# Performance work log

Hardware: AMD Instinct MI355X
Metric: run time of the kernel (lower is better)

## Reference

```python
import jax, jax.numpy as jnp
import numpy as np

B, T, D = 2, 4096, 512
H, W = 8, 32
HD = D // H            # 64
HIDDEN = 3 * D         # SwiGLU expansion = 3
SCALE = float(np.sqrt(HD))
EPS = 1e-5


def setup_inputs() -> dict:
    key = jax.random.key(0)
    ks = jax.random.split(key, 8)
    s = 0.02  # small init for weight matrices
    return {
        "x": jax.random.normal(ks[0], (B, T, D), dtype=jnp.float32),
        "pre_g": jnp.ones((D,), jnp.float32), "pre_b": jnp.zeros((D,), jnp.float32),
        "wq": jax.random.normal(ks[1], (D, D), jnp.float32) * s,
        "wkv": jax.random.normal(ks[2], (D, 2 * D), jnp.float32) * s,
        "wo": jax.random.normal(ks[3], (D, D), jnp.float32) * s,
        "attn_g": jnp.ones((D,), jnp.float32), "attn_b": jnp.zeros((D,), jnp.float32),
        "freqs": jax.random.normal(ks[4], (D,), jnp.float32) * 0.02,
        "phases": jnp.zeros((D,), jnp.float32),
        "amp": jnp.full((1,), 0.1, jnp.float32),
        "w_gate": jax.random.normal(ks[5], (D, HIDDEN), jnp.float32) * s,
        "w_val": jax.random.normal(ks[6], (D, HIDDEN), jnp.float32) * s,
        "w_proj": jax.random.normal(ks[7], (HIDDEN, D), jnp.float32) * s,
        "ffn_g": jnp.ones((D,), jnp.float32), "ffn_b": jnp.zeros((D,), jnp.float32),
    }


def _ln(x, g, b):
    mu = jnp.mean(x, axis=-1, keepdims=True)
    var = jnp.mean(jnp.square(x - mu), axis=-1, keepdims=True)
    return (x - mu) * jax.lax.rsqrt(var + EPS) * g + b


def _gather_window(z):
    # z: (B, T, H, C) -> nb: (B, T, W, H, C) with nb[:, t, w] = z[:, t-1-w] (zeros if t-1-w < 0)
    zp = jnp.pad(z, ((0, 0), (W, 0), (0, 0), (0, 0)))
    idx = jnp.arange(T)[:, None] + (W - 1) - jnp.arange(W)[None, :]  # (T, W), values in [0, T+W-1)
    return zp[:, idx]  # (B, T, W, H, C)


def reference(x, pre_g, pre_b, wq, wkv, wo, attn_g, attn_b,
              freqs, phases, amp, w_gate, w_val, w_proj, ffn_g, ffn_b):
    h = _ln(x, pre_g, pre_b)

    # ---- multi-head causal tension (sigmoid local attention) ----
    q = (h @ wq).reshape(B, T, H, HD)
    kv = (h @ wkv).reshape(B, T, H, 2 * HD)
    nb_kv = _gather_window(kv)                     # (B, T, W, H, 2*HD)
    nb_k, nb_v = nb_kv[..., :HD], nb_kv[..., HD:]
    tau = jax.nn.sigmoid(jnp.einsum('bthd,btwhd->bthw', q, nb_k) / SCALE)
    msg = jnp.einsum('bthw,btwhd->bthd', tau, nb_v).reshape(B, T, D)
    h = _ln(h + msg @ wo, attn_g, attn_b)

    # ---- oscillatory modulation ----
    pos = jnp.arange(T, dtype=jnp.float32)[:, None]  # (T, 1)
    mod = jnp.sin(pos * freqs + phases)              # (T, D)
    y = h * (1.0 + amp * mod)[None]

    # ---- SwiGLU FFN ----
    z = (jax.nn.silu(y @ w_gate) * (y @ w_val)) @ w_proj
    return _ln(y + z, ffn_g, ffn_b)
```

## Files before the change

### kernel.cpp

```cpp
#include <hip/hip_runtime.h>
#include <hip/hip_bf16.h>
#include <math.h>

#define T_LEN   4096
#define D_DIM   512
#define H_NUM   8
#define HD_DIM  64
#define W_WIN   32
#define HID_DIM 1536
#define M_ROWS  8192
#define QKV_LD  1536
#define BK 64

typedef __hip_bfloat16 bf16;
typedef __bf16  bf16x8 __attribute__((ext_vector_type(8)));
typedef float   f32x4  __attribute__((ext_vector_type(4)));

#define G_AS __attribute__((address_space(1)))
#define L_AS __attribute__((address_space(3)))

#define SBAR()        __builtin_amdgcn_s_barrier()
#define SCHED_FENCE() __builtin_amdgcn_sched_barrier(0)
#define WAIT_VM(N)    asm volatile("s_waitcnt vmcnt(" #N ")" ::: "memory")
#define WAIT_LGKM0()  asm volatile("s_waitcnt lgkmcnt(0)" ::: "memory")

__device__ __forceinline__ float b2f(bf16 x) { return __bfloat162float(x); }
__device__ __forceinline__ bf16  f2b(float x){ return __float2bfloat16(x); }

__device__ __forceinline__ void gload_lds16(const bf16* g, bf16* l) {
  __builtin_amdgcn_global_load_lds((const G_AS unsigned int*)g,
                                   (L_AS unsigned int*)l, 16, 0, 0);
}

__device__ __forceinline__ float rdP(const void* p, int i, bool f32) {
  return f32 ? ((const float*)p)[i] : b2f(((const bf16*)p)[i]);
}

__device__ __forceinline__ float wave_reduce_sum(float v) {
  #pragma unroll
  for (int off = 32; off; off >>= 1) v += __shfl_xor(v, off, 64);
  return v;
}

__device__ __forceinline__ bool detect_f32(const unsigned* __restrict__ x) {
  int lane = threadIdx.x & 63;
  int votes = 0;
  #pragma unroll
  for (int i = 0; i < 4; ++i) {
    unsigned e = (x[lane * 4 + i] >> 7) & 0xffu;
    votes += (e >= 90u && e <= 140u) ? 1 : 0;
  }
  float v = wave_reduce_sum((float)votes);
  return v < 200.f;
}

__device__ __forceinline__ void swizzle_xy(int gx, int& bx, int& by) {
  int lid = blockIdx.x;
  int sub = lid & 7;
  int grp = lid >> 3;
  bx = grp % gx;
  by = (grp / gx) * 8 + sub;
}

__global__ __launch_bounds__(256) void ln_kernel(
    const void* __restrict__ in, const void* __restrict__ g, const void* __restrict__ bb,
    void* __restrict__ out, int mode,
    const void* __restrict__ freqs, const void* __restrict__ phases,
    const void* __restrict__ amp,
    const unsigned* __restrict__ xdet, int in_follows, int out_follows)
{
  bool f32  = detect_f32(xdet);
  bool inF  = f32 && (in_follows != 0);
  bool outF = f32 && (out_follows != 0);

  int wave = threadIdx.x >> 6;
  int lane = threadIdx.x & 63;
  int row  = blockIdx.x * 4 + wave;

  float x[8];
  if (inF) {
    const float* rp = (const float*)in + (size_t)row * D_DIM + lane * 8;
    float4 v0 = *reinterpret_cast<const float4*>(rp);
    float4 v1 = *reinterpret_cast<const float4*>(rp + 4);
    x[0]=v0.x; x[1]=v0.y; x[2]=v0.z; x[3]=v0.w;
    x[4]=v1.x; x[5]=v1.y; x[6]=v1.z; x[7]=v1.w;
  } else {
    bf16x8 v = *reinterpret_cast<const bf16x8*>(
        (const bf16*)in + (size_t)row * D_DIM + lane * 8);
    #pragma unroll
    for (int i = 0; i < 8; ++i) x[i] = (float)v[i];
  }

  float s = 0.f, s2 = 0.f;
  #pragma unroll
  for (int i = 0; i < 8; ++i) { s += x[i]; s2 += x[i]*x[i]; }
  s  = wave_reduce_sum(s);
  s2 = wave_reduce_sum(s2);
  float mu   = s * (1.f / D_DIM);
  float var  = s2 * (1.f / D_DIM) - mu * mu;
  float rstd = rsqrtf(var + 1e-5f);

  int t = row & (T_LEN - 1);
  float ampf = (mode == 1) ? rdP(amp, 0, f32) : 0.f;

  float o[8];
  #pragma unroll
  for (int i = 0; i < 8; ++i) {
    int d = lane * 8 + i;
    float val = (x[i] - mu) * rstd * rdP(g, d, f32) + rdP(bb, d, f32);
    if (mode == 1) {
      float m = sinf(fmaf((float)t, rdP(freqs, d, f32), rdP(phases, d, f32)));
      val *= (1.f + ampf * m);
    }
    o[i] = val;
  }

  if (outF) {
    float* op = (float*)out + (size_t)row * D_DIM + lane * 8;
    *reinterpret_cast<float4*>(op)     = make_float4(o[0], o[1], o[2], o[3]);
    *reinterpret_cast<float4*>(op + 4) = make_float4(o[4], o[5], o[6], o[7]);
  } else {
    bf16x8 ov;
    #pragma unroll
    for (int i = 0; i < 8; ++i) ov[i] = (__bf16)o[i];
    *reinterpret_cast<bf16x8*>((bf16*)out + (size_t)row * D_DIM + lane * 8) = ov;
  }
}

__global__ __launch_bounds__(256) void prep_kernel(
    const void* s0, const void* s1, const void* s2, const void* s3,
    const void* s4, const void* s5,
    bf16* d0, bf16* d1, bf16* d2, bf16* d3, bf16* d4, bf16* d5,
    const void* __restrict__ xin, const void* __restrict__ pre_g,
    const void* __restrict__ pre_b, bf16* __restrict__ hout,
    const unsigned* __restrict__ xdet)
{
  __shared__ bf16 tile[32][33];
  bool f32 = detect_f32(xdet);
  int bid = blockIdx.x;

  if (bid >= 3328) {
    int wave = threadIdx.x >> 6;
    int lane = threadIdx.x & 63;
    int row  = (bid - 3328) * 4 + wave;

    float x[8];
    if (f32) {
      const float* rp = (const float*)xin + (size_t)row * D_DIM + lane * 8;
      float4 v0 = *reinterpret_cast<const float4*>(rp);
      float4 v1 = *reinterpret_cast<const float4*>(rp + 4);
      x[0]=v0.x; x[1]=v0.y; x[2]=v0.z; x[3]=v0.w;
      x[4]=v1.x; x[5]=v1.y; x[6]=v1.z; x[7]=v1.w;
    } else {
      bf16x8 v = *reinterpret_cast<const bf16x8*>(
          (const bf16*)xin + (size_t)row * D_DIM + lane * 8);
      #pragma unroll
      for (int i = 0; i < 8; ++i) x[i] = (float)v[i];
    }

    float s = 0.f, s2 = 0.f;
    #pragma unroll
    for (int i = 0; i < 8; ++i) { s += x[i]; s2 += x[i]*x[i]; }
    s  = wave_reduce_sum(s);
    s2 = wave_reduce_sum(s2);
    float mu   = s * (1.f / D_DIM);
    float var  = s2 * (1.f / D_DIM) - mu * mu;
    float rstd = rsqrtf(var + 1e-5f);

    bf16x8 ov;
    #pragma unroll
    for (int i = 0; i < 8; ++i) {
      int d = lane * 8 + i;
      ov[i] = (__bf16)((x[i] - mu) * rstd * rdP(pre_g, d, f32) + rdP(pre_b, d, f32));
    }
    *reinterpret_cast<bf16x8*>(hout + (size_t)row * D_DIM + lane * 8) = ov;
    return;
  }

  const void* src; bf16* dst; int R, C, lid, tiles_x;
  if      (bid < 256)  { src=s0; dst=d0; R=512;  C=512;  lid=bid;      tiles_x=16; }
  else if (bid < 768)  { src=s1; dst=d1; R=512;  C=1024; lid=bid-256;  tiles_x=32; }
  else if (bid < 1024) { src=s2; dst=d2; R=512;  C=512;  lid=bid-768;  tiles_x=16; }
  else if (bid < 1792) { src=s3; dst=d3; R=512;  C=1536; lid=bid-1024; tiles_x=48; }
  else if (bid < 2560) { src=s4; dst=d4; R=512;  C=1536; lid=bid-1792; tiles_x=48; }
  else                 { src=s5; dst=d5; R=1536; C=512;  lid=bid-2560; tiles_x=16; }

  int tx = threadIdx.x & 31;
  int ty = threadIdx.x >> 5;
  int c0 = (lid % tiles_x) * 32;
  int r0 = (lid / tiles_x) * 32;
  #pragma unroll
  for (int j = 0; j < 32; j += 8)
    tile[ty + j][tx] = f2b(rdP(src, (size_t)(r0 + ty + j) * C + c0 + tx, f32));
  __syncthreads();
  #pragma unroll
  for (int j = 0; j < 32; j += 8)
    dst[(size_t)(c0 + ty + j) * R + r0 + tx] = tile[tx][ty + j];
}

template<int BNT, bool DBUF>
__global__ __launch_bounds__(256) void gemm_tile_kernel(
    const bf16* __restrict__ A, const bf16* __restrict__ Bt,
    bf16* Cout, const bf16* extra, int N, int K, int lda, int mode, int gx)
{
  constexpr int BJ  = BNT / 32;
  constexpr int NB  = DBUF ? 2 : 1;
  constexpr int ASZ = 128 * BK;
  constexpr int BSZ = BNT * BK;
  constexpr int CPF = BNT + 4;
  constexpr int CPB = BNT + 8;
  constexpr size_t STAGE = (size_t)NB * (ASZ + BSZ) * 2;
  constexpr size_t CTSZ  = (BNT == 64) ? (size_t)128 * CPF * 4 : (size_t)128 * CPB * 2;
  constexpr size_t SMEMSZ = STAGE > CTSZ ? STAGE : CTSZ;
  __shared__ alignas(16) char smem[SMEMSZ];
  bf16* Asb = (bf16*)smem;
  bf16* Bsb = Asb + (size_t)NB * ASZ;

  int bx, by; swizzle_xy(gx, bx, by);
  int mbase = by * 128, nbase = bx * BNT;
  int tid  = threadIdx.x;
  int lane = tid & 63;
  int wid  = tid >> 6;
  int quad = lane >> 4, l16 = lane & 15;
  int wm = (wid >> 1) * 64, wn = (wid & 1) * (BNT / 2);

  int srow = tid >> 3;
  int scol = (tid & 7) ^ (srow & 7);
  const bf16* Ag = A  + (size_t)(mbase + srow) * lda + scol * 8;
  const bf16* Bg = Bt + (size_t)(nbase + srow) * K   + scol * 8;

  f32x4 acc[4][BJ] = {};
  int nk = K / BK;

  auto compute = [&](int cb) {
    #pragma unroll
    for (int ko = 0; ko < 2; ++ko) {
      bf16x8 a[4], b[BJ];
      int c = ((ko * 4 + quad) ^ (l16 & 7)) * 8;
      #pragma unroll
      for (int i = 0; i < 4; ++i)
        a[i] = *reinterpret_cast<const bf16x8*>(&Asb[cb * ASZ + (wm + i * 16 + l16) * BK + c]);
      #pragma unroll
      for (int j = 0; j < BJ; ++j)
        b[j] = *reinterpret_cast<const bf16x8*>(&Bsb[cb * BSZ + (wn + j * 16 + l16) * BK + c]);
      #pragma unroll
      for (int i = 0; i < 4; ++i)
        #pragma unroll
        for (int j = 0; j < BJ; ++j)
          acc[i][j] = __builtin_amdgcn_mfma_f32_16x16x32_bf16(a[i], b[j], acc[i][j], 0, 0, 0);
    }
  };

  if constexpr (DBUF) {
    #pragma unroll
    for (int j = 0; j < 4; ++j)
      gload_lds16(Ag + (size_t)(j * 32) * lda, &Asb[j * 2048 + tid * 8]);
    #pragma unroll
    for (int j = 0; j < BJ; ++j)
      gload_lds16(Bg + (size_t)(j * 32) * K,   &Bsb[j * 2048 + tid * 8]);
    Ag += BK; Bg += BK;

    for (int t = 0; t < nk; ++t) {
      int cur = t & 1;
      if (t + 1 < nk) {
        int nxt = cur ^ 1;
        #pragma unroll
        for (int j = 0; j < 4; ++j)
          gload_lds16(Ag + (size_t)(j * 32) * lda, &Asb[nxt * ASZ + j * 2048 + tid * 8]);
        #pragma unroll
        for (int j = 0; j < BJ; ++j)
          gload_lds16(Bg + (size_t)(j * 32) * K,   &Bsb[nxt * BSZ + j * 2048 + tid * 8]);
        Ag += BK; Bg += BK;
        if constexpr (BNT == 128) { WAIT_VM(8); } else { WAIT_VM(6); }
      } else {
        WAIT_VM(0);
      }
      SBAR();
      SCHED_FENCE();

      compute(cur);

      WAIT_LGKM0();
      SBAR();
      SCHED_FENCE();
    }
  } else {
    for (int t = 0; t < nk; ++t) {
      __syncthreads();
      #pragma unroll
      for (int j = 0; j < 4; ++j)
        gload_lds16(Ag + (size_t)(j * 32) * lda, &Asb[j * 2048 + tid * 8]);
      #pragma unroll
      for (int j = 0; j < BJ; ++j)
        gload_lds16(Bg + (size_t)(j * 32) * K,   &Bsb[j * 2048 + tid * 8]);
      Ag += BK; Bg += BK;
      __syncthreads();

      compute(0);
    }
    __syncthreads();
  }

  if constexpr (BNT == 64) {
    float* CT = (float*)smem;
    #pragma unroll
    for (int i = 0; i < 4; ++i)
      #pragma unroll
      for (int j = 0; j < 2; ++j)
        #pragma unroll
        for (int r = 0; r < 4; ++r)
          CT[(wm + i * 16 + quad * 4 + r) * CPF + wn + j * 16 + l16] = acc[i][j][r];
    __syncthreads();
    #pragma unroll
    for (int p = 0; p < 4; ++p) {
      int row = (tid >> 3) + p * 32;
      int c8  = tid & 7;
      const float* rp = &CT[row * CPF + c8 * 8];
      float4 v0 = *reinterpret_cast<const float4*>(rp);
      float4 v1 = *reinterpret_cast<const float4*>(rp + 4);
      float vv[8] = {v0.x, v0.y, v0.z, v0.w, v1.x, v1.y, v1.z, v1.w};
      size_t gidx = (size_t)(mbase + row) * N + nbase + c8 * 8;
      if (mode == 1) {
        bf16x8 e = *reinterpret_cast<const bf16x8*>(extra + gidx);
        #pragma unroll
        for (int k2 = 0; k2 < 8; ++k2) vv[k2] += (float)e[k2];
      }
      bf16x8 ov;
      #pragma unroll
      for (int k2 = 0; k2 < 8; ++k2) ov[k2] = (__bf16)vv[k2];
      *reinterpret_cast<bf16x8*>(Cout + gidx) = ov;
    }
  } else {
    bf16* CT = (bf16*)smem;
    #pragma unroll
    for (int i = 0; i < 4; ++i)
      #pragma unroll
      for (int j = 0; j < BJ; ++j)
        #pragma unroll
        for (int r = 0; r < 4; ++r)
          CT[(wm + i * 16 + quad * 4 + r) * CPB + wn + j * 16 + l16] = f2b(acc[i][j][r]);
    __syncthreads();
    #pragma unroll
    for (int p = 0; p < 8; ++p) {
      int row = (tid >> 4) + p * 16;
      int c16 = tid & 15;
      bf16x8 ov = *reinterpret_cast<const bf16x8*>(&CT[row * CPB + c16 * 8]);
      *reinterpret_cast<bf16x8*>(Cout + (size_t)(mbase + row) * N + nbase + c16 * 8) = ov;
    }
  }
}

__global__ __launch_bounds__(256) void gateval_kernel(
    const bf16* __restrict__ A, const bf16* __restrict__ Btg,
    const bf16* __restrict__ Btv, bf16* __restrict__ Cout,
    int N, int K, int lda, int gx)
{
  constexpr int CP = 72;
  __shared__ alignas(16) char smem[2 * (16384 + 8192 + 8192)];
  bf16* Asb = (bf16*)smem;
  bf16* Bgs = Asb + 2 * 8192;
  bf16* Bvs = Bgs + 2 * 4096;

  int bx, by; swizzle_xy(gx, bx, by);
  int mbase = by * 128, nbase = bx * 64;
  int tid  = threadIdx.x;
  int lane = tid & 63;
  int wid  = tid >> 6;
  int quad = lane >> 4, l16 = lane & 15;
  int wm = (wid >> 1) * 64, wn = (wid & 1) * 32;

  int srow = tid >> 3;
  int scol = (tid & 7) ^ (srow & 7);
  const bf16* Ag = A   + (size_t)(mbase + srow) * lda + scol * 8;
  const bf16* Gg = Btg + (size_t)(nbase + srow) * K   + scol * 8;
  const bf16* Vg = Btv + (size_t)(nbase + srow) * K   + scol * 8;

  f32x4 accg[4][2] = {};
  f32x4 accv[4][2] = {};
  int nk = K / BK;

  #pragma unroll
  for (int j = 0; j < 4; ++j)
    gload_lds16(Ag + (size_t)(j * 32) * lda, &Asb[j * 2048 + tid * 8]);
  #pragma unroll
  for (int j = 0; j < 2; ++j) {
    gload_lds16(Gg + (size_t)(j * 32) * K, &Bgs[j * 2048 + tid * 8]);
    gload_lds16(Vg + (size_t)(j * 32) * K, &Bvs[j * 2048 + tid * 8]);
  }
  Ag += BK; Gg += BK; Vg += BK;

  for (int t = 0; t < nk; ++t) {
    int cur = t & 1;
    if (t + 1 < nk) {
      int nxt = cur ^ 1;
      #pragma unroll
      for (int j = 0; j < 4; ++j)
        gload_lds16(Ag + (size_t)(j * 32) * lda, &Asb[nxt * 8192 + j * 2048 + tid * 8]);
      #pragma unroll
      for (int j = 0; j < 2; ++j) {
        gload_lds16(Gg + (size_t)(j * 32) * K, &Bgs[nxt * 4096 + j * 2048 + tid * 8]);
        gload_lds16(Vg + (size_t)(j * 32) * K, &Bvs[nxt * 4096 + j * 2048 + tid * 8]);
      }
      Ag += BK; Gg += BK; Vg += BK;
      WAIT_VM(8);
    } else {
      WAIT_VM(0);
    }
    SBAR();
    SCHED_FENCE();

    #pragma unroll
    for (int ko = 0; ko < 2; ++ko) {
      bf16x8 a[4], bg[2], bv[2];
      int c = ((ko * 4 + quad) ^ (l16 & 7)) * 8;
      #pragma unroll
      for (int i = 0; i < 4; ++i)
        a[i]  = *reinterpret_cast<const bf16x8*>(&Asb[cur * 8192 + (wm + i * 16 + l16) * BK + c]);
      #pragma unroll
      for (int j = 0; j < 2; ++j) {
        bg[j] = *reinterpret_cast<const bf16x8*>(&Bgs[cur * 4096 + (wn + j * 16 + l16) * BK + c]);
        bv[j] = *reinterpret_cast<const bf16x8*>(&Bvs[cur * 4096 + (wn + j * 16 + l16) * BK + c]);
      }
      #pragma unroll
      for (int i = 0; i < 4; ++i)
        #pragma unroll
        for (int j = 0; j < 2; ++j) {
          accg[i][j] = __builtin_amdgcn_mfma_f32_16x16x32_bf16(a[i], bg[j], accg[i][j], 0, 0, 0);
          accv[i][j] = __builtin_amdgcn_mfma_f32_16x16x32_bf16(a[i], bv[j], accv[i][j], 0, 0, 0);
        }
    }

    WAIT_LGKM0();
    SBAR();
    SCHED_FENCE();
  }

  bf16* CT = (bf16*)smem;
  #pragma unroll
  for (int i = 0; i < 4; ++i)
    #pragma unroll
    for (int j = 0; j < 2; ++j)
      #pragma unroll
      for (int r = 0; r < 4; ++r) {
        float g = accg[i][j][r];
        float v = accv[i][j][r];
        CT[(wm + i * 16 + quad * 4 + r) * CP + wn + j * 16 + l16] =
            f2b(g / (1.f + expf(-g)) * v);
      }
  __syncthreads();
  #pragma unroll
  for (int p = 0; p < 4; ++p) {
    int row = (tid >> 3) + p * 32;
    int c8  = tid & 7;
    bf16x8 ov = *reinterpret_cast<const bf16x8*>(&CT[row * CP + c8 * 8]);
    *reinterpret_cast<bf16x8*>(Cout + (size_t)(mbase + row) * N + nbase + c8 * 8) = ov;
  }
}

#define VT_BYTES 9216
#define PL_BYTES 2304
#define ATTN_SET (VT_BYTES + PL_BYTES)
__device__ __forceinline__ int vt_addr(int d, int t) { return d * 144 + t * 2; }

__global__ __launch_bounds__(256) void attn_mfma_kernel(bf16* qkv)
{
  __shared__ alignas(16) char lds_raw[4 * ATTN_SET];
  int lane = threadIdx.x & 63;
  int widx = threadIdx.x >> 6;
  int u    = blockIdx.x * 4 + widx;
  int tile = u >> 3, head = u & 7;
  int rowbase = tile * 16;
  int t0   = rowbase & (T_LEN - 1);
  int l16  = lane & 15, quad = lane >> 4;

  char* wbase = lds_raw + widx * ATTN_SET;
  char* Vl = wbase;
  bf16* Pl = (bf16*)(wbase + VT_BYTES);

  #pragma unroll
  for (int it = 0; it < 6; ++it) {
    int chunk = it * 64 + lane;
    int t  = chunk >> 3;
    int dc = chunk & 7;
    int row = rowbase - 32 + t;
    if (row < 0) row = 0;
    bf16x8 v = *reinterpret_cast<const bf16x8*>(
        qkv + (size_t)row * QKV_LD + 512 + head * 128 + 64 + dc * 8);
    #pragma unroll
    for (int jj = 0; jj < 8; ++jj)
      *(bf16*)(Vl + vt_addr(dc * 8 + jj, t)) = (bf16)(__bf16)v[jj];
  }
  bf16x8 z = {};
  *reinterpret_cast<bf16x8*>(Vl + vt_addr(lane, 48)) = z;
  *reinterpret_cast<bf16x8*>(Vl + vt_addr(lane, 56)) = z;

  bf16x8 aq0, aq1;
  {
    const bf16* qrow = qkv + (size_t)(rowbase + l16) * QKV_LD + head * HD_DIM + quad * 8;
    aq0 = *reinterpret_cast<const bf16x8*>(qrow);
    aq1 = *reinterpret_cast<const bf16x8*>(qrow + 32);
  }

  f32x4 sacc[3] = {};
  #pragma unroll
  for (int jt = 0; jt < 3; ++jt) {
    int tok = rowbase - 32 + jt * 16 + l16;
    if (tok < 0) tok = 0;
    const bf16* krow = qkv + (size_t)tok * QKV_LD + 512 + head * 128 + quad * 8;
    bf16x8 b0 = *reinterpret_cast<const bf16x8*>(krow);
    bf16x8 b1 = *reinterpret_cast<const bf16x8*>(krow + 32);
    sacc[jt] = __builtin_amdgcn_mfma_f32_16x16x32_bf16(aq0, b0, sacc[jt], 0, 0, 0);
    sacc[jt] = __builtin_amdgcn_mfma_f32_16x16x32_bf16(aq1, b1, sacc[jt], 0, 0, 0);
  }

  #pragma unroll
  for (int jt = 0; jt < 3; ++jt) {
    int j = jt * 16 + l16;
    #pragma unroll
    for (int r = 0; r < 4; ++r) {
      int i = quad * 4 + r;
      bool valid = (j >= i) && (j <= i + 31) && (t0 - 32 + j >= 0);
      float tau = valid ? 1.f / (1.f + expf(-sacc[jt][r] * 0.125f)) : 0.f;
      Pl[i * 72 + j] = f2b(tau);
    }
  }
  #pragma unroll
  for (int r = 0; r < 4; ++r) Pl[(quad * 4 + r) * 72 + 48 + l16] = f2b(0.f);

  __syncthreads();

  bf16x8 ap0 = *reinterpret_cast<const bf16x8*>((char*)Pl + l16 * 144 + quad * 16);
  bf16x8 ap1 = *reinterpret_cast<const bf16x8*>((char*)Pl + l16 * 144 + 64 + quad * 16);

  f32x4 macc[4] = {};
  #pragma unroll
  for (int nt = 0; nt < 4; ++nt) {
    int d = nt * 16 + l16;
    bf16x8 bv0 = *reinterpret_cast<const bf16x8*>(Vl + vt_addr(d, quad * 8));
    bf16x8 bv1 = *reinterpret_cast<const bf16x8*>(Vl + vt_addr(d, 32 + quad * 8));
    macc[nt] = __builtin_amdgcn_mfma_f32_16x16x32_bf16(ap0, bv0, macc[nt], 0, 0, 0);
    macc[nt] = __builtin_amdgcn_mfma_f32_16x16x32_bf16(ap1, bv1, macc[nt], 0, 0, 0);
  }

  #pragma unroll
  for (int nt = 0; nt < 4; ++nt)
    #pragma unroll
    for (int r = 0; r < 4; ++r)
      Pl[(quad * 4 + r) * 72 + nt * 16 + l16] = f2b(macc[nt][r]);

  #pragma unroll
  for (int p = 0; p < 2; ++p) {
    int row = (lane >> 3) + p * 8;
    int c8  = lane & 7;
    bf16x8 ov = *reinterpret_cast<const bf16x8*>(&Pl[row * 72 + c8 * 8]);
    *reinterpret_cast<bf16x8*>(
        qkv + (size_t)(rowbase + row) * QKV_LD + head * HD_DIM + c8 * 8) = ov;
  }
}

extern "C" void kernel_launch(void* const* d_in, const int* in_sizes, int n_in,
                              void* d_out, int out_size, void* d_ws, size_t ws_size,
                              hipStream_t stream)
{
  const void* x      = d_in[0];
  const void* pre_g  = d_in[1];
  const void* pre_b  = d_in[2];
  const void* wq     = d_in[3];
  const void* wkv    = d_in[4];
  const void* wo     = d_in[5];
  const void* attn_g = d_in[6];
  const void* attn_b = d_in[7];
  const void* freqs  = d_in[8];
  const void* phases = d_in[9];
  const void* amp    = d_in[10];
  const void* w_gate = d_in[11];
  const void* w_val  = d_in[12];
  const void* w_proj = d_in[13];
  const void* ffn_g  = d_in[14];
  const void* ffn_b  = d_in[15];
  const unsigned* xdet = (const unsigned*)x;

  char* ws = (char*)d_ws;
  bf16* Btqkv = (bf16*)(ws + 512);
  bf16* Bto   = (bf16*)(ws + 1573376);
  bf16* Btg   = (bf16*)(ws + 2097664);
  bf16* Btv   = (bf16*)(ws + 3670528);
  bf16* Btp   = (bf16*)(ws + 5243392);
  bf16* h     = (bf16*)(ws + 6816256);
  bf16* qkvb  = (bf16*)(ws + 15204864);
  bf16* gb    = qkvb;

  prep_kernel<<<5376, 256, 0, stream>>>(
      wq, wkv, wo, w_gate, w_val, w_proj,
      Btqkv, Btqkv + 512 * 512, Bto, Btg, Btv, Btp,
      x, pre_g, pre_b, h, xdet);

  gemm_tile_kernel<128, false><<<768, 256, 0, stream>>>(h, Btqkv, qkvb, nullptr,
                                                        1536, 512, 512, 0, 12);

  attn_mfma_kernel<<<1024, 256, 0, stream>>>(qkvb);

  gemm_tile_kernel<64, true><<<512, 256, 0, stream>>>(qkvb, Bto, h, h,
                                                      512, 512, QKV_LD, 1, 8);

  ln_kernel<<<2048, 256, 0, stream>>>(h, attn_g, attn_b, h, 1,
                                      freqs, phases, amp, xdet, 0, 0);

  gateval_kernel<<<1536, 256, 0, stream>>>(h, Btg, Btv, gb,
                                           1536, 512, 512, 24);

  gemm_tile_kernel<64, true><<<512, 256, 0, stream>>>(gb, Btp, h, h,
                                                      512, 1536, QKV_LD, 1, 8);

  ln_kernel<<<2048, 256, 0, stream>>>(h, ffn_g, ffn_b, d_out, 0,
                                      nullptr, nullptr, nullptr, xdet, 0, 1);
}
```

Measured before the change: 274.3 us.

## Use 512-thread blocks for GEMM kernels and switch to fast sine

The GEMM and gate/value kernels now run with 512 threads (8 waves) per block on the same output tile. Each wave gets a smaller sub-tile with fewer accumulators, and the global-to-LDS staging and epilogue loops are re-split so each thread issues fewer loads. The aim is more waves in flight to hide memory latency and lower register pressure, at the cost of less reuse per wave and more LDS reads per MFMA. The oscillatory modulation also swaps sinf for __sinf, which is cheaper but less accurate when t*freq is large.

```diff
diff --git a/kernel.cpp b/kernel.cpp
--- a/kernel.cpp
+++ b/kernel.cpp
@@ -109,7 +109,7 @@
     int d = lane * 8 + i;
     float val = (x[i] - mu) * rstd * rdP(g, d, f32) + rdP(bb, d, f32);
     if (mode == 1) {
-      float m = sinf(fmaf((float)t, rdP(freqs, d, f32), rdP(phases, d, f32)));
+      float m = __sinf(fmaf((float)t, rdP(freqs, d, f32), rdP(phases, d, f32)));
       val *= (1.f + ampf * m);
     }
     o[i] = val;
@@ -199,16 +199,17 @@
 }
 
 template<int BNT, bool DBUF>
-__global__ __launch_bounds__(256) void gemm_tile_kernel(
+__global__ __launch_bounds__(512) void gemm_tile_kernel(
     const bf16* __restrict__ A, const bf16* __restrict__ Bt,
     bf16* Cout, const bf16* extra, int N, int K, int lda, int mode, int gx)
 {
-  constexpr int BJ  = BNT / 32;
+  constexpr int MI  = (BNT == 128) ? 4 : 2;
+  constexpr int NJ  = 2;
   constexpr int NB  = DBUF ? 2 : 1;
   constexpr int ASZ = 128 * BK;
   constexpr int BSZ = BNT * BK;
-  constexpr int CPF = BNT + 4;
-  constexpr int CPB = BNT + 8;
+  constexpr int CPF = 68;
+  constexpr int CPB = 136;
   constexpr size_t STAGE = (size_t)NB * (ASZ + BSZ) * 2;
   constexpr size_t CTSZ  = (BNT == 64) ? (size_t)128 * CPF * 4 : (size_t)128 * CPB * 2;
   constexpr size_t SMEMSZ = STAGE > CTSZ ? STAGE : CTSZ;
@@ -222,56 +223,56 @@
   int lane = tid & 63;
   int wid  = tid >> 6;
   int quad = lane >> 4, l16 = lane & 15;
-  int wm = (wid >> 1) * 64, wn = (wid & 1) * (BNT / 2);
-
-  int srow = tid >> 3;
-  int scol = (tid & 7) ^ (srow & 7);
-  const bf16* Ag = A  + (size_t)(mbase + srow) * lda + scol * 8;
-  const bf16* Bg = Bt + (size_t)(nbase + srow) * K   + scol * 8;
-
-  f32x4 acc[4][BJ] = {};
+  int wm, wn;
+  if constexpr (BNT == 128) { wm = (wid >> 2) * 64; wn = (wid & 3) * 32; }
+  else                      { wm = (wid >> 1) * 32; wn = (wid & 1) * 32; }
+
+  int srow  = tid >> 3;
+  int scolb = ((tid & 7) ^ (srow & 7)) * 8;
+  const bf16* Ag = A  + (size_t)(mbase + srow) * lda + scolb;
+  const bf16* Bg = Bt + (size_t)(nbase + srow) * K   + scolb;
+
+  f32x4 acc[MI][NJ] = {};
   int nk = K / BK;
 
+  auto stage = [&](int buf) {
+    gload_lds16(Ag,                    &Asb[buf * ASZ + tid * 8]);
+    gload_lds16(Ag + (size_t)64 * lda, &Asb[buf * ASZ + tid * 8 + 4096]);
+    if constexpr (BNT == 128) {
+      gload_lds16(Bg,                  &Bsb[buf * BSZ + tid * 8]);
+      gload_lds16(Bg + (size_t)64 * K, &Bsb[buf * BSZ + tid * 8 + 4096]);
+    } else {
+      gload_lds16(Bg,                  &Bsb[buf * BSZ + tid * 8]);
+    }
+    Ag += BK; Bg += BK;
+  };
+
   auto compute = [&](int cb) {
     #pragma unroll
     for (int ko = 0; ko < 2; ++ko) {
-      bf16x8 a[4], b[BJ];
+      bf16x8 a[MI], b[NJ];
       int c = ((ko * 4 + quad) ^ (l16 & 7)) * 8;
       #pragma unroll
-      for (int i = 0; i < 4; ++i)
+      for (int i = 0; i < MI; ++i)
         a[i] = *reinterpret_cast<const bf16x8*>(&Asb[cb * ASZ + (wm + i * 16 + l16) * BK + c]);
       #pragma unroll
-      for (int j = 0; j < BJ; ++j)
+      for (int j = 0; j < NJ; ++j)
         b[j] = *reinterpret_cast<const bf16x8*>(&Bsb[cb * BSZ + (wn + j * 16 + l16) * BK + c]);
       #pragma unroll
-      for (int i = 0; i < 4; ++i)
+      for (int i = 0; i < MI; ++i)
         #pragma unroll
-        for (int j = 0; j < BJ; ++j)
+        for (int j = 0; j < NJ; ++j)
           acc[i][j] = __builtin_amdgcn_mfma_f32_16x16x32_bf16(a[i], b[j], acc[i][j], 0, 0, 0);
     }
   };
 
   if constexpr (DBUF) {
-    #pragma unroll
-    for (int j = 0; j < 4; ++j)
-      gload_lds16(Ag + (size_t)(j * 32) * lda, &Asb[j * 2048 + tid * 8]);
-    #pragma unroll
-    for (int j = 0; j < BJ; ++j)
-      gload_lds16(Bg + (size_t)(j * 32) * K,   &Bsb[j * 2048 + tid * 8]);
-    Ag += BK; Bg += BK;
-
+    stage(0);
     for (int t = 0; t < nk; ++t) {
       int cur = t & 1;
       if (t + 1 < nk) {
-        int nxt = cur ^ 1;
-        #pragma unroll
-        for (int j = 0; j < 4; ++j)
-          gload_lds16(Ag + (size_t)(j * 32) * lda, &Asb[nxt * ASZ + j * 2048 + tid * 8]);
-        #pragma unroll
-        for (int j = 0; j < BJ; ++j)
-          gload_lds16(Bg + (size_t)(j * 32) * K,   &Bsb[nxt * BSZ + j * 2048 + tid * 8]);
-        Ag += BK; Bg += BK;
-        if constexpr (BNT == 128) { WAIT_VM(8); } else { WAIT_VM(6); }
+        stage(cur ^ 1);
+        if constexpr (BNT == 128) { WAIT_VM(4); } else { WAIT_VM(3); }
       } else {
         WAIT_VM(0);
       }
@@ -287,15 +288,8 @@
   } else {
     for (int t = 0; t < nk; ++t) {
       __syncthreads();
-      #pragma unroll
-      for (int j = 0; j < 4; ++j)
-        gload_lds16(Ag + (size_t)(j * 32) * lda, &Asb[j * 2048 + tid * 8]);
-      #pragma unroll
-      for (int j = 0; j < BJ; ++j)
-        gload_lds16(Bg + (size_t)(j * 32) * K,   &Bsb[j * 2048 + tid * 8]);
-      Ag += BK; Bg += BK;
+      stage(0);
       __syncthreads();
-
       compute(0);
     }
     __syncthreads();
@@ -304,16 +298,16 @@
   if constexpr (BNT == 64) {
     float* CT = (float*)smem;
     #pragma unroll
-    for (int i = 0; i < 4; ++i)
-      #pragma unroll
-      for (int j = 0; j < 2; ++j)
+    for (int i = 0; i < MI; ++i)
+      #pragma unroll
+      for (int j = 0; j < NJ; ++j)
         #pragma unroll
         for (int r = 0; r < 4; ++r)
           CT[(wm + i * 16 + quad * 4 + r) * CPF + wn + j * 16 + l16] = acc[i][j][r];
     __syncthreads();
     #pragma unroll
-    for (int p = 0; p < 4; ++p) {
-      int row = (tid >> 3) + p * 32;
+    for (int p = 0; p < 2; ++p) {
+      int row = (tid >> 3) + p * 64;
       int c8  = tid & 7;
       const float* rp = &CT[row * CPF + c8 * 8];
       float4 v0 = *reinterpret_cast<const float4*>(rp);
@@ -333,16 +327,16 @@
   } else {
     bf16* CT = (bf16*)smem;
     #pragma unroll
-    for (int i = 0; i < 4; ++i)
-      #pragma unroll
-      for (int j = 0; j < BJ; ++j)
+    for (int i = 0; i < MI; ++i)
+      #pragma unroll
+      for (int j = 0; j < NJ; ++j)
         #pragma unroll
         for (int r = 0; r < 4; ++r)
           CT[(wm + i * 16 + quad * 4 + r) * CPB + wn + j * 16 + l16] = f2b(acc[i][j][r]);
     __syncthreads();
     #pragma unroll
-    for (int p = 0; p < 8; ++p) {
-      int row = (tid >> 4) + p * 16;
+    for (int p = 0; p < 4; ++p) {
+      int row = (tid >> 4) + p * 32;
       int c16 = tid & 15;
       bf16x8 ov = *reinterpret_cast<const bf16x8*>(&CT[row * CPB + c16 * 8]);
       *reinterpret_cast<bf16x8*>(Cout + (size_t)(mbase + row) * N + nbase + c16 * 8) = ov;
@@ -350,7 +344,7 @@
   }
 }
 
-__global__ __launch_bounds__(256) void gateval_kernel(
+__global__ __launch_bounds__(512) void gateval_kernel(
     const bf16* __restrict__ A, const bf16* __restrict__ Btg,
     const bf16* __restrict__ Btv, bf16* __restrict__ Cout,
     int N, int K, int lda, int gx)
@@ -367,42 +361,32 @@
   int lane = tid & 63;
   int wid  = tid >> 6;
   int quad = lane >> 4, l16 = lane & 15;
-  int wm = (wid >> 1) * 64, wn = (wid & 1) * 32;
-
-  int srow = tid >> 3;
-  int scol = (tid & 7) ^ (srow & 7);
-  const bf16* Ag = A   + (size_t)(mbase + srow) * lda + scol * 8;
-  const bf16* Gg = Btg + (size_t)(nbase + srow) * K   + scol * 8;
-  const bf16* Vg = Btv + (size_t)(nbase + srow) * K   + scol * 8;
-
-  f32x4 accg[4][2] = {};
-  f32x4 accv[4][2] = {};
+  int wm = (wid >> 1) * 32, wn = (wid & 1) * 32;
+
+  int srow  = tid >> 3;
+  int scolb = ((tid & 7) ^ (srow & 7)) * 8;
+  const bf16* Ag = A   + (size_t)(mbase + srow) * lda + scolb;
+  const bf16* Gg = Btg + (size_t)(nbase + srow) * K   + scolb;
+  const bf16* Vg = Btv + (size_t)(nbase + srow) * K   + scolb;
+
+  f32x4 accg[2][2] = {};
+  f32x4 accv[2][2] = {};
   int nk = K / BK;
 
-  #pragma unroll
-  for (int j = 0; j < 4; ++j)
-    gload_lds16(Ag + (size_t)(j * 32) * lda, &Asb[j * 2048 + tid * 8]);
-  #pragma unroll
-  for (int j = 0; j < 2; ++j) {
-    gload_lds16(Gg + (size_t)(j * 32) * K, &Bgs[j * 2048 + tid * 8]);
-    gload_lds16(Vg + (size_t)(j * 32) * K, &Bvs[j * 2048 + tid * 8]);
-  }
-  Ag += BK; Gg += BK; Vg += BK;
-
+  auto stage = [&](int buf) {
+    gload_lds16(Ag,                    &Asb[buf * 8192 + tid * 8]);
+    gload_lds16(Ag + (size_t)64 * lda, &Asb[buf * 8192 + tid * 8 + 4096]);
+    gload_lds16(Gg,                    &Bgs[buf * 4096 + tid * 8]);
+    gload_lds16(Vg,                    &Bvs[buf * 4096 + tid * 8]);
+    Ag += BK; Gg += BK; Vg += BK;
+  };
+
+  stage(0);
   for (int t = 0; t < nk; ++t) {
     int cur = t & 1;
     if (t + 1 < nk) {
-      int nxt = cur ^ 1;
-      #pragma unroll
-      for (int j = 0; j < 4; ++j)
-        gload_lds16(Ag + (size_t)(j * 32) * lda, &Asb[nxt * 8192 + j * 2048 + tid * 8]);
-      #pragma unroll
-      for (int j = 0; j < 2; ++j) {
-        gload_lds16(Gg + (size_t)(j * 32) * K, &Bgs[nxt * 4096 + j * 2048 + tid * 8]);
-        gload_lds16(Vg + (size_t)(j * 32) * K, &Bvs[nxt * 4096 + j * 2048 + tid * 8]);
-      }
-      Ag += BK; Gg += BK; Vg += BK;
-      WAIT_VM(8);
+      stage(cur ^ 1);
+      WAIT_VM(4);
     } else {
       WAIT_VM(0);
     }
@@ -411,10 +395,10 @@
 
     #pragma unroll
     for (int ko = 0; ko < 2; ++ko) {
-      bf16x8 a[4], bg[2], bv[2];
+      bf16x8 a[2], bg[2], bv[2];
       int c = ((ko * 4 + quad) ^ (l16 & 7)) * 8;
       #pragma unroll
-      for (int i = 0; i < 4; ++i)
+      for (int i = 0; i < 2; ++i)
         a[i]  = *reinterpret_cast<const bf16x8*>(&Asb[cur * 8192 + (wm + i * 16 + l16) * BK + c]);
       #pragma unroll
       for (int j = 0; j < 2; ++j) {
@@ -422,7 +406,7 @@
         bv[j] = *reinterpret_cast<const bf16x8*>(&Bvs[cur * 4096 + (wn + j * 16 + l16) * BK + c]);
       }
       #pragma unroll
-      for (int i = 0; i < 4; ++i)
+      for (int i = 0; i < 2; ++i)
         #pragma unroll
         for (int j = 0; j < 2; ++j) {
           accg[i][j] = __builtin_amdgcn_mfma_f32_16x16x32_bf16(a[i], bg[j], accg[i][j], 0, 0, 0);
@@ -437,7 +421,7 @@
 
   bf16* CT = (bf16*)smem;
   #pragma unroll
-  for (int i = 0; i < 4; ++i)
+  for (int i = 0; i < 2; ++i)
     #pragma unroll
     for (int j = 0; j < 2; ++j)
       #pragma unroll
@@ -449,8 +433,8 @@
       }
   __syncthreads();
   #pragma unroll
-  for (int p = 0; p < 4; ++p) {
-    int row = (tid >> 3) + p * 32;
+  for (int p = 0; p < 2; ++p) {
+    int row = (tid >> 3) + p * 64;
     int c8  = tid & 7;
     bf16x8 ov = *reinterpret_cast<const bf16x8*>(&CT[row * CP + c8 * 8]);
     *reinterpret_cast<bf16x8*>(Cout + (size_t)(mbase + row) * N + nbase + c8 * 8) = ov;
@@ -595,21 +579,21 @@
       Btqkv, Btqkv + 512 * 512, Bto, Btg, Btv, Btp,
       x, pre_g, pre_b, h, xdet);
 
-  gemm_tile_kernel<128, false><<<768, 256, 0, stream>>>(h, Btqkv, qkvb, nullptr,
+  gemm_tile_kernel<128, false><<<768, 512, 0, stream>>>(h, Btqkv, qkvb, nullptr,
                                                         1536, 512, 512, 0, 12);
 
   attn_mfma_kernel<<<1024, 256, 0, stream>>>(qkvb);
 
-  gemm_tile_kernel<64, true><<<512, 256, 0, stream>>>(qkvb, Bto, h, h,
+  gemm_tile_kernel<64, true><<<512, 512, 0, stream>>>(qkvb, Bto, h, h,
                                                       512, 512, QKV_LD, 1, 8);
 
   ln_kernel<<<2048, 256, 0, stream>>>(h, attn_g, attn_b, h, 1,
                                       freqs, phases, amp, xdet, 0, 0);
 
-  gateval_kernel<<<1536, 256, 0, stream>>>(h, Btg, Btv, gb,
+  gateval_kernel<<<1536, 512, 0, stream>>>(h, Btg, Btv, gb,
                                            1536, 512, 512, 24);
 
-  gemm_tile_kernel<64, true><<<512, 256, 0, stream>>>(gb, Btp, h, h,
+  gemm_tile_kernel<64, true><<<512, 512, 0, stream>>>(gb, Btp, h, h,
                                                       512, 1536, QKV_LD, 1, 8);
 
   ln_kernel<<<2048, 256, 0, stream>>>(h, ffn_g, ffn_b, d_out, 0,
```

Measured after the change: 263.9 us. 1.04x faster.
